# Kernel optimization log

Hardware: AMD Instinct MI355X
Metric: run time of the kernel (lower is better)

## Reference

```python
import jax, jax.numpy as jnp
import numpy as np

B, T, C = 8, 2048, 1024   # batch, seq_len, n_embd
HS = 1024                 # head_size


def setup_inputs() -> dict:
    key = jax.random.key(0)
    k1, k2, k3, k4 = jax.random.split(key, 4)
    x = jax.random.normal(k1, (B, T, C), dtype=jnp.float32)
    k_wei = jax.random.normal(k2, (C, HS), dtype=jnp.float32) * (C ** -0.5)
    q_wei = jax.random.normal(k3, (C, HS), dtype=jnp.float32) * (C ** -0.5)
    v_wei = jax.random.normal(k4, (C, HS), dtype=jnp.float32) * (C ** -0.5)
    mask = jnp.tril(jnp.ones((T, T), dtype=bool))  # causal tril, block_size >= T
    return {"x": x, "k_wei": k_wei, "q_wei": q_wei, "v_wei": v_wei, "mask": mask}


def reference(x, k_wei, q_wei, v_wei, mask):
    Bb, Tt, Cc = x.shape
    k = x @ k_wei                                   # [B,T,HS]
    q = x @ q_wei                                   # [B,T,HS]
    v = x @ v_wei                                   # [B,T,HS]
    # NOTE: source scales by C**-0.5 where C = n_embd (input channels)
    wei = jnp.einsum('bqh,bkh->bqk', q, k) * (Cc ** -0.5)  # [B,T,T]
    wei = jnp.where(mask[:Tt, :Tt], wei, -jnp.inf)
    wei = jax.nn.softmax(wei, axis=-1)
    out = wei @ v                                   # [B,T,HS]
    return out
```

## Files before the change

### kernel.cpp

```cpp
#include <hip/hip_runtime.h>
#include <hip/hip_bf16.h>
#include <stdint.h>

typedef __attribute__((ext_vector_type(4))) float f32x4;
typedef __attribute__((ext_vector_type(8))) short s16x8;

#define MFMA(a, b, c) __builtin_amdgcn_mfma_f32_16x16x32_bf16((a), (b), (c), 0, 0, 0)

__device__ __forceinline__ ushort f2bf(float f) {
  union { float f; uint32_t u; } v; v.f = f;
  uint32_t r = v.u + 0x7FFFu + ((v.u >> 16) & 1u);
  return (ushort)(r >> 16);
}

__device__ __forceinline__ void gload_lds16(const ushort* g, short* l) {
  __builtin_amdgcn_global_load_lds(
      (const __attribute__((address_space(1))) uint32_t*)g,
      (__attribute__((address_space(3))) uint32_t*)l, 16, 0, 0);
}

__device__ __forceinline__ int xcd_swz(int flat, int q) {
  return (flat & 7) * q + (flat >> 3);
}

__device__ __forceinline__ void stage128(const ushort* __restrict__ g, int ld,
                                         int row0, int k0, short* lbase, int tid) {
  const int w  = tid >> 6;
  const int l  = tid & 63;
  const int lr = l >> 3;
  const int ls = l & 7;
  const ushort* gp = g + (size_t)(row0 + lr) * ld + k0 + ((ls ^ lr) << 3);
  short* lp = lbase + l * 8;
#pragma unroll
  for (int i = 0; i < 4; ++i) {
    const int R0 = w * 32 + i * 8;
    gload_lds16(gp + (size_t)R0 * ld, lp + R0 * 64);
  }
}

__device__ __forceinline__ void gemm_core(
    const ushort* __restrict__ A, int lda, const ushort* __restrict__ Bt, int ldb,
    int m0, int n0, int nk, short* lds, f32x4 acc[4][4])
{
  const int tid  = threadIdx.x;
  const int lane = tid & 63, wid = tid >> 6;
  const int wr = wid >> 1, wc = wid & 1;
  const int fr = lane & 15, kg = lane >> 4;
  const int s0  = (kg ^ (fr & 7)) << 3;
  const int aro = (wr * 64 + fr) * 64;
  const int bro = (wc * 64 + fr) * 64;

  short* As = lds;
  short* Bs = lds + 8192;

#pragma unroll
  for (int i = 0; i < 4; ++i)
#pragma unroll
    for (int j = 0; j < 4; ++j)
      acc[i][j] = (f32x4){0.f, 0.f, 0.f, 0.f};

#pragma unroll 1
  for (int kk = 0; kk < nk; ++kk) {
    __syncthreads();
    stage128(A,  lda, m0, kk * 64, As, tid);
    stage128(Bt, ldb, n0, kk * 64, Bs, tid);
    __syncthreads();

    s16x8 b[4][2], a[2][2];
#pragma unroll
    for (int ni = 0; ni < 4; ++ni) {
      b[ni][0] = *(const s16x8*)(Bs + bro + ni * 1024 + s0);
      b[ni][1] = *(const s16x8*)(Bs + bro + ni * 1024 + (s0 ^ 32));
    }
#pragma unroll
    for (int mi = 0; mi < 2; ++mi) {
      a[mi][0] = *(const s16x8*)(As + aro + mi * 1024 + s0);
      a[mi][1] = *(const s16x8*)(As + aro + mi * 1024 + (s0 ^ 32));
    }
#pragma unroll
    for (int mi = 0; mi < 2; ++mi)
#pragma unroll
      for (int ni = 0; ni < 4; ++ni) {
        acc[mi][ni] = MFMA(a[mi][0], b[ni][0], acc[mi][ni]);
        acc[mi][ni] = MFMA(a[mi][1], b[ni][1], acc[mi][ni]);
      }
#pragma unroll
    for (int mi = 0; mi < 2; ++mi) {
      a[mi][0] = *(const s16x8*)(As + aro + (2 + mi) * 1024 + s0);
      a[mi][1] = *(const s16x8*)(As + aro + (2 + mi) * 1024 + (s0 ^ 32));
    }
#pragma unroll
    for (int mi = 0; mi < 2; ++mi)
#pragma unroll
      for (int ni = 0; ni < 4; ++ni) {
        acc[2 + mi][ni] = MFMA(a[mi][0], b[ni][0], acc[2 + mi][ni]);
        acc[2 + mi][ni] = MFMA(a[mi][1], b[ni][1], acc[2 + mi][ni]);
      }
  }
}

__global__ void cvt_x(const float* __restrict__ x, ushort* __restrict__ xb)
{
  const size_t i = (size_t)(blockIdx.x * 256 + threadIdx.x) * 4;
  const f32x4 t = *(const f32x4*)(x + i);
  uint2 pk;
  pk.x = (uint32_t)f2bf(t[0]) | ((uint32_t)f2bf(t[1]) << 16);
  pk.y = (uint32_t)f2bf(t[2]) | ((uint32_t)f2bf(t[3]) << 16);
  *(uint2*)(xb + i) = pk;
}

__global__ void cvt_w(const float* __restrict__ kw, const float* __restrict__ qw,
                      const float* __restrict__ vw, ushort* __restrict__ wt)
{
  __shared__ float t[32][33];
  const float* w = (blockIdx.z == 0) ? qw : (blockIdx.z == 1) ? kw : vw;
  const int n0 = blockIdx.x * 32, k0 = blockIdx.y * 32;
  t[threadIdx.y][threadIdx.x] = w[(size_t)(k0 + threadIdx.y) * 1024 + n0 + threadIdx.x];
  __syncthreads();
  wt[(size_t)blockIdx.z * 1048576 + (size_t)(n0 + threadIdx.y) * 1024 + k0 + threadIdx.x] =
      f2bf(t[threadIdx.x][threadIdx.y]);
}

__global__ __launch_bounds__(256, 4) void gemm_qkv_impl(
    const ushort* __restrict__ xb, const ushort* __restrict__ wt,
    ushort* __restrict__ q, ushort* __restrict__ k, ushort* __restrict__ vT)
{
  __attribute__((aligned(16))) __shared__ short lds[16384];
  const int flat = blockIdx.x + 24 * blockIdx.y;
  const int xcd = flat & 7, c = flat >> 3;
  const int mloc = c / 6, nloc = c - mloc * 6;
  const int m0 = ((xcd & 1) * 64 + mloc) * 128;
  const int n0 = ((xcd >> 1) * 6 + nloc) * 128;
  f32x4 acc[4][4];
  gemm_core(xb, 1024, wt, 1024, m0, n0, 16, lds, acc);

  const int lane = threadIdx.x & 63;
  const int wid = threadIdx.x >> 6;
  const int wr = wid >> 1, wc = wid & 1;
  const int q4 = (lane >> 4) << 2;
  const int fr = lane & 15;
  const int z  = n0 >> 10;
  const int cb = (n0 & 1023) + wc * 64 + fr;
  ushort* o = (z == 0) ? q : k;
#pragma unroll
  for (int mi = 0; mi < 4; ++mi)
#pragma unroll
    for (int ni = 0; ni < 4; ++ni)
#pragma unroll
      for (int j = 0; j < 4; ++j) {
        const int r = m0 + wr * 64 + mi * 16 + q4 + j;
        const int c2 = cb + ni * 16;
        const ushort hv = f2bf(acc[mi][ni][j]);
        if (z < 2) o[(size_t)r * 1024 + c2] = hv;
        else       vT[((size_t)(r >> 11) * 1024 + c2) * 2048 + (r & 2047)] = hv;
      }
}

__global__ __launch_bounds__(256, 4) void gemm_sp(
    const ushort* __restrict__ q, const ushort* __restrict__ k,
    ushort* __restrict__ P, float* __restrict__ sums)
{
  __attribute__((aligned(16))) __shared__ short lds[16384];
  const int nf = xcd_swz(blockIdx.x + 16 * (blockIdx.y + 16 * blockIdx.z), 256);
  const int kt = nf & 15, qt = (nf >> 4) & 15, b = nf >> 8;
  if (kt > qt) return;
  f32x4 acc[4][4];
  const ushort* qb = q + (size_t)b * (2048 * 1024);
  const ushort* kb = k + (size_t)b * (2048 * 1024);
  gemm_core(qb, 1024, kb, 1024, qt * 128, kt * 128, 16, lds, acc);
  __syncthreads();
  float* rowsum = (float*)lds;

  const int tid  = threadIdx.x;
  const int lane = tid & 63, wid = tid >> 6;
  const int wr = wid >> 1, wc = wid & 1;
  const int q4 = (lane >> 4) << 2;
  const int fr = lane & 15;
  const int diag = (kt == qt);
  ushort* Pb = P + ((size_t)b << 22);

#pragma unroll
  for (int mi = 0; mi < 4; ++mi)
#pragma unroll
    for (int j = 0; j < 4; ++j) {
      const int rloc = wr * 64 + mi * 16 + q4 + j;
      const int rg   = qt * 128 + rloc;
      float s = 0.f;
#pragma unroll
      for (int ni = 0; ni < 4; ++ni) {
        const int cg = kt * 128 + wc * 64 + ni * 16 + fr;
        float e = __expf(acc[mi][ni][j] * 0.03125f - 10.f);
        if (diag && cg > rg) e = 0.f;
        s += e;
        Pb[(size_t)rg * 2048 + cg] = f2bf(e);
      }
#pragma unroll
      for (int m = 1; m < 16; m <<= 1) s += __shfl_xor(s, m);
      if (fr == 0) rowsum[wc * 128 + rloc] = s;
    }
  __syncthreads();
  if (tid < 128) {
    const float tot = rowsum[tid] + rowsum[128 + tid];
    atomicAdd(&sums[b * 2048 + qt * 128 + tid], tot);
  }
}

__global__ __launch_bounds__(256, 4) void gemm_pv(
    const ushort* __restrict__ P, const ushort* __restrict__ vT,
    const float* __restrict__ sums, float* __restrict__ out)
{
  __attribute__((aligned(16))) __shared__ short lds[16384];
  const int nf = xcd_swz(blockIdx.x + 8 * (blockIdx.y + 16 * blockIdx.z), 128);
  const int ht = nf & 7, qt = (nf >> 3) & 15, b = nf >> 7;
  f32x4 acc[4][4];
  const ushort* Pb = P  + ((size_t)b << 22);
  const ushort* Vb = vT + (size_t)b * (1024 * 2048);
  gemm_core(Pb, 2048, Vb, 2048, qt * 128, ht * 128, (qt + 1) * 2, lds, acc);

  float* ob = out + (size_t)b * 2097152;
  const int lane = threadIdx.x & 63;
  const int wid = threadIdx.x >> 6;
  const int wr = wid >> 1, wc = wid & 1;
  const int r0 = qt * 128 + wr * 64 + ((lane >> 4) << 2);
  const int c0 = ht * 128 + wc * 64 + (lane & 15);
#pragma unroll
  for (int mi = 0; mi < 4; ++mi)
#pragma unroll
    for (int j = 0; j < 4; ++j) {
      const int r = r0 + mi * 16 + j;
      const float inv = 1.0f / sums[b * 2048 + r];
#pragma unroll
      for (int ni = 0; ni < 4; ++ni)
        ob[(size_t)r * 1024 + (c0 + ni * 16)] = acc[mi][ni][j] * inv;
    }
}

extern "C" void kernel_launch(void* const* d_in, const int* in_sizes, int n_in,
                              void* d_out, int out_size, void* d_ws, size_t ws_size,
                              hipStream_t stream)
{
  const float* x  = (const float*)d_in[0];
  const float* kw = (const float*)d_in[1];
  const float* qw = (const float*)d_in[2];
  const float* vw = (const float*)d_in[3];
  float* out = (float*)d_out;
  char* ws = (char*)d_ws;

  ushort* xb   = (ushort*)ws;
  ushort* P    = (ushort*)ws;
  float*  sums = (float*)(ws + 67108864);
  ushort* wt   = (ushort*)(ws + 67174400);
  ushort* q    = (ushort*)(ws + 73465856);
  ushort* k    = (ushort*)(ws + 107020288);
  ushort* vT   = (ushort*)(ws + 140574720);

  hipMemsetAsync(sums, 0, 8 * 2048 * sizeof(float), stream);
  cvt_x<<<16384, 256, 0, stream>>>(x, xb);
  cvt_w<<<dim3(32, 32, 3), dim3(32, 32), 0, stream>>>(kw, qw, vw, wt);
  gemm_qkv_impl<<<dim3(24, 128), 256, 0, stream>>>(xb, wt, q, k, vT);
  gemm_sp<<<dim3(16, 16, 8), 256, 0, stream>>>(q, k, P, sums);
  gemm_pv<<<dim3(8, 16, 8), 256, 0, stream>>>(P, vT, sums, out);
}
```

Measured before the change: 294.3 us.

## Use 256x256 tile with 8-wave pingpong pipeline for QKV projection GEMM

Replaces the 128x128, 4-wave QKV projection GEMM with a 256x256 tile computed by 512 threads (8 waves) using 128KB of dynamic LDS. Global-to-LDS loads run double-buffered and are interleaved with quarter-tile MFMA phases, using explicit barriers, vmcnt waits and setprio. The aim is more operand reuse per loaded byte and better overlap of memory traffic with MFMA work. The cost is lower occupancy (one block per CU), far fewer blocks (768), and many barriers per iteration.

```diff
diff --git a/kernel.cpp b/kernel.cpp
--- a/kernel.cpp
+++ b/kernel.cpp
@@ -5,6 +5,11 @@
 typedef __attribute__((ext_vector_type(4))) float f32x4;
 typedef __attribute__((ext_vector_type(8))) short s16x8;
 
+#define BARRIER() asm volatile("s_barrier" ::: "memory")
+#define WAITV8()  asm volatile("s_waitcnt vmcnt(8)" ::: "memory")
+#define WAITV4()  asm volatile("s_waitcnt vmcnt(4)" ::: "memory")
+#define WAITV0()  asm volatile("s_waitcnt vmcnt(0)" ::: "memory")
+#define LGKM0()   asm volatile("s_waitcnt lgkmcnt(0)" ::: "memory")
 #define MFMA(a, b, c) __builtin_amdgcn_mfma_f32_16x16x32_bf16((a), (b), (c), 0, 0, 0)
 
 __device__ __forceinline__ ushort f2bf(float f) {
@@ -22,6 +27,7 @@
 __device__ __forceinline__ int xcd_swz(int flat, int q) {
   return (flat & 7) * q + (flat >> 3);
 }
+
 
 __device__ __forceinline__ void stage128(const ushort* __restrict__ g, int ld,
                                          int row0, int k0, short* lbase, int tid) {
@@ -99,6 +105,162 @@
   }
 }
 
+
+__device__ __forceinline__ void stage_half(const ushort* __restrict__ g, int ld,
+                                           int grow0, int k0, short* lbase, int tid) {
+#pragma unroll
+  for (int i = 0; i < 2; ++i) {
+    const int idx = i * 512 + tid;
+    const int r = idx >> 3;
+    const int s = tid & 7;
+    gload_lds16(g + (size_t)(grow0 + r) * ld + k0 + ((s ^ (r & 7)) << 3),
+                lbase + idx * 8);
+  }
+}
+
+#define QMFMA(mbase, nbase, bq)                                              \
+  __builtin_amdgcn_s_setprio(1);                                             \
+  _Pragma("unroll")                                                          \
+  for (int m = 0; m < 4; ++m) {                                              \
+    _Pragma("unroll")                                                        \
+    for (int n = 0; n < 2; ++n) {                                            \
+      acc[(mbase) + m][(nbase) + n] =                                        \
+          MFMA(a[m][0], bq[n][0], acc[(mbase) + m][(nbase) + n]);            \
+      acc[(mbase) + m][(nbase) + n] =                                        \
+          MFMA(a[m][1], bq[n][1], acc[(mbase) + m][(nbase) + n]);            \
+    }                                                                        \
+  }                                                                          \
+  __builtin_amdgcn_s_setprio(0);
+
+__device__ __forceinline__ void gemm_core256(
+    const ushort* __restrict__ A, int lda, const ushort* __restrict__ Bt, int ldb,
+    int m0, int n0, int nk, short* lds, f32x4 acc[8][4])
+{
+  const int tid  = threadIdx.x;
+  const int lane = tid & 63, wid = tid >> 6;
+  const int wr = wid >> 2, wc = wid & 3;
+  const int fr = lane & 15, kg = lane >> 4;
+  const int s0  = (kg ^ (fr & 7)) << 3;
+  const int aro = fr * 64;
+  const int bro = (wc & 1) * 4096 + fr * 64;
+
+#define ASL(s, h) (lds + ((s) * 2 + (h)) * 8192)
+#define BSL(s, h) (lds + 32768 + ((s) * 2 + (h)) * 8192)
+  short* const Aw[2] = { ASL(0, wr), ASL(1, wr) };
+  short* const Bw[2] = { BSL(0, (wc >> 1)), BSL(1, (wc >> 1)) };
+
+#pragma unroll
+  for (int i = 0; i < 8; ++i)
+#pragma unroll
+    for (int j = 0; j < 4; ++j)
+      acc[i][j] = (f32x4){0.f, 0.f, 0.f, 0.f};
+
+  stage_half(A,  lda, m0,       0,  ASL(0, 0), tid);
+  stage_half(A,  lda, m0 + 128, 0,  ASL(0, 1), tid);
+  stage_half(Bt, ldb, n0,       0,  BSL(0, 0), tid);
+  stage_half(Bt, ldb, n0 + 128, 0,  BSL(0, 1), tid);
+  stage_half(A,  lda, m0,       64, ASL(1, 0), tid);
+  stage_half(A,  lda, m0 + 128, 64, ASL(1, 1), tid);
+  stage_half(Bt, ldb, n0,       64, BSL(1, 0), tid);
+  stage_half(Bt, ldb, n0 + 128, 64, BSL(1, 1), tid);
+  WAITV8();
+  BARRIER();
+
+  const int niter = nk >> 1;
+#pragma unroll 1
+  for (int t = 0; t < niter; ++t) {
+    const int kO  = (2 * t + 1) * 64;
+    const int kN0 = (2 * t + 2) * 64;
+    const int kN1 = (2 * t + 3) * 64;
+    const bool more = (t + 1 < niter);
+    s16x8 a[4][2], b01[2][2], b23[2][2];
+
+#pragma unroll
+    for (int n = 0; n < 2; ++n) {
+      b01[n][0] = *(const s16x8*)(Bw[0] + bro + n * 1024 + s0);
+      b01[n][1] = *(const s16x8*)(Bw[0] + bro + n * 1024 + (s0 ^ 32));
+    }
+#pragma unroll
+    for (int m = 0; m < 4; ++m) {
+      a[m][0] = *(const s16x8*)(Aw[0] + aro + m * 1024 + s0);
+      a[m][1] = *(const s16x8*)(Aw[0] + aro + m * 1024 + (s0 ^ 32));
+    }
+    if (t > 0) stage_half(A, lda, m0 + 128, kO, ASL(1, 1), tid);
+    BARRIER(); LGKM0();
+    QMFMA(0, 0, b01);
+    BARRIER();
+
+#pragma unroll
+    for (int n = 0; n < 2; ++n) {
+      b23[n][0] = *(const s16x8*)(Bw[0] + bro + (2 + n) * 1024 + s0);
+      b23[n][1] = *(const s16x8*)(Bw[0] + bro + (2 + n) * 1024 + (s0 ^ 32));
+    }
+    if (t > 0) stage_half(Bt, ldb, n0 + 128, kO, BSL(1, 1), tid);
+    BARRIER(); LGKM0();
+    QMFMA(0, 2, b23);
+    BARRIER();
+
+#pragma unroll
+    for (int m = 0; m < 4; ++m) {
+      a[m][0] = *(const s16x8*)(Aw[0] + aro + (4 + m) * 1024 + s0);
+      a[m][1] = *(const s16x8*)(Aw[0] + aro + (4 + m) * 1024 + (s0 ^ 32));
+    }
+    if (more) stage_half(Bt, ldb, n0, kN0, BSL(0, 0), tid);
+    BARRIER(); LGKM0();
+    QMFMA(4, 2, b23);
+    BARRIER();
+
+    if (more) stage_half(A, lda, m0, kN0, ASL(0, 0), tid);
+    BARRIER();
+    QMFMA(4, 0, b01);
+    if (more) { WAITV4(); } else { WAITV0(); }
+    BARRIER();
+
+#pragma unroll
+    for (int n = 0; n < 2; ++n) {
+      b01[n][0] = *(const s16x8*)(Bw[1] + bro + n * 1024 + s0);
+      b01[n][1] = *(const s16x8*)(Bw[1] + bro + n * 1024 + (s0 ^ 32));
+    }
+#pragma unroll
+    for (int m = 0; m < 4; ++m) {
+      a[m][0] = *(const s16x8*)(Aw[1] + aro + m * 1024 + s0);
+      a[m][1] = *(const s16x8*)(Aw[1] + aro + m * 1024 + (s0 ^ 32));
+    }
+    if (more) stage_half(A, lda, m0 + 128, kN0, ASL(0, 1), tid);
+    BARRIER(); LGKM0();
+    QMFMA(0, 0, b01);
+    BARRIER();
+
+#pragma unroll
+    for (int n = 0; n < 2; ++n) {
+      b23[n][0] = *(const s16x8*)(Bw[1] + bro + (2 + n) * 1024 + s0);
+      b23[n][1] = *(const s16x8*)(Bw[1] + bro + (2 + n) * 1024 + (s0 ^ 32));
+    }
+    if (more) stage_half(Bt, ldb, n0 + 128, kN0, BSL(0, 1), tid);
+    BARRIER(); LGKM0();
+    QMFMA(0, 2, b23);
+    BARRIER();
+
+#pragma unroll
+    for (int m = 0; m < 4; ++m) {
+      a[m][0] = *(const s16x8*)(Aw[1] + aro + (4 + m) * 1024 + s0);
+      a[m][1] = *(const s16x8*)(Aw[1] + aro + (4 + m) * 1024 + (s0 ^ 32));
+    }
+    if (more) stage_half(Bt, ldb, n0, kN1, BSL(1, 0), tid);
+    BARRIER(); LGKM0();
+    QMFMA(4, 2, b23);
+    BARRIER();
+
+    if (more) stage_half(A, lda, m0, kN1, ASL(1, 0), tid);
+    BARRIER();
+    QMFMA(4, 0, b01);
+    if (more) { WAITV4(); } else { WAITV0(); }
+    BARRIER();
+  }
+#undef ASL
+#undef BSL
+}
+
 __global__ void cvt_x(const float* __restrict__ x, ushort* __restrict__ xb)
 {
   const size_t i = (size_t)(blockIdx.x * 256 + threadIdx.x) * 4;
@@ -121,34 +283,34 @@
       f2bf(t[threadIdx.x][threadIdx.y]);
 }
 
-__global__ __launch_bounds__(256, 4) void gemm_qkv_impl(
+__global__ __launch_bounds__(512) void gemm_qkv256(
     const ushort* __restrict__ xb, const ushort* __restrict__ wt,
     ushort* __restrict__ q, ushort* __restrict__ k, ushort* __restrict__ vT)
 {
-  __attribute__((aligned(16))) __shared__ short lds[16384];
-  const int flat = blockIdx.x + 24 * blockIdx.y;
+  extern __shared__ short lds[];
+  const int flat = blockIdx.x + 12 * blockIdx.y;
   const int xcd = flat & 7, c = flat >> 3;
-  const int mloc = c / 6, nloc = c - mloc * 6;
-  const int m0 = ((xcd & 1) * 64 + mloc) * 128;
-  const int n0 = ((xcd >> 1) * 6 + nloc) * 128;
-  f32x4 acc[4][4];
-  gemm_core(xb, 1024, wt, 1024, m0, n0, 16, lds, acc);
+  const int mloc = c / 3, nloc = c - mloc * 3;
+  const int m0 = ((xcd & 1) * 32 + mloc) * 256;
+  const int n0 = ((xcd >> 1) * 3 + nloc) * 256;
+  f32x4 acc[8][4];
+  gemm_core256(xb, 1024, wt, 1024, m0, n0, 16, lds, acc);
 
   const int lane = threadIdx.x & 63;
   const int wid = threadIdx.x >> 6;
-  const int wr = wid >> 1, wc = wid & 1;
+  const int wr = wid >> 2, wc = wid & 3;
   const int q4 = (lane >> 4) << 2;
   const int fr = lane & 15;
   const int z  = n0 >> 10;
   const int cb = (n0 & 1023) + wc * 64 + fr;
   ushort* o = (z == 0) ? q : k;
 #pragma unroll
-  for (int mi = 0; mi < 4; ++mi)
+  for (int mi = 0; mi < 8; ++mi)
 #pragma unroll
     for (int ni = 0; ni < 4; ++ni)
 #pragma unroll
       for (int j = 0; j < 4; ++j) {
-        const int r = m0 + wr * 64 + mi * 16 + q4 + j;
+        const int r = m0 + wr * 128 + mi * 16 + q4 + j;
         const int c2 = cb + ni * 16;
         const ushort hv = f2bf(acc[mi][ni][j]);
         if (z < 2) o[(size_t)r * 1024 + c2] = hv;
@@ -254,10 +416,13 @@
   ushort* k    = (ushort*)(ws + 107020288);
   ushort* vT   = (ushort*)(ws + 140574720);
 
+  const int LDSB = 131072;
+  hipFuncSetAttribute((const void*)gemm_qkv256, hipFuncAttributeMaxDynamicSharedMemorySize, LDSB);
+
   hipMemsetAsync(sums, 0, 8 * 2048 * sizeof(float), stream);
   cvt_x<<<16384, 256, 0, stream>>>(x, xb);
   cvt_w<<<dim3(32, 32, 3), dim3(32, 32), 0, stream>>>(kw, qw, vw, wt);
-  gemm_qkv_impl<<<dim3(24, 128), 256, 0, stream>>>(xb, wt, q, k, vT);
+  gemm_qkv256<<<dim3(12, 64), 512, LDSB, stream>>>(xb, wt, q, k, vT);
   gemm_sp<<<dim3(16, 16, 8), 256, 0, stream>>>(q, k, P, sums);
   gemm_pv<<<dim3(8, 16, 8), 256, 0, stream>>>(P, vT, sums, out);
 }
```

After: 293.0 us. Within noise of the previous version (-0.4%).

## Load QKV GEMM A-operand directly to registers with double-buffered LDS for B

Applied to the files above, without the earlier changes.

The QKV projection GEMM stops staging the activation tile through LDS. Each wave now loads its A fragments straight from global memory into registers, prefetching one k-step ahead. Only the weight tile stays in LDS, double-buffered with asynchronous global-to-LDS loads issued two steps ahead and explicit vmcnt waits. This removes half the LDS traffic and overlaps loads with MFMA work, at the cost of more registers, uncoalesced-ish direct global reads, and dropping the occupancy hint from the launch bounds.

```diff
diff --git a/kernel.cpp b/kernel.cpp
--- a/kernel.cpp
+++ b/kernel.cpp
@@ -5,6 +5,9 @@
 typedef __attribute__((ext_vector_type(4))) float f32x4;
 typedef __attribute__((ext_vector_type(8))) short s16x8;
 
+#define BARRIER() asm volatile("s_barrier" ::: "memory")
+#define WAITV4()  asm volatile("s_waitcnt vmcnt(4)" ::: "memory")
+#define WAITV0()  asm volatile("s_waitcnt vmcnt(0)" ::: "memory")
 #define MFMA(a, b, c) __builtin_amdgcn_mfma_f32_16x16x32_bf16((a), (b), (c), 0, 0, 0)
 
 __device__ __forceinline__ ushort f2bf(float f) {
@@ -38,6 +41,7 @@
   }
 }
 
+
 __device__ __forceinline__ void gemm_core(
     const ushort* __restrict__ A, int lda, const ushort* __restrict__ Bt, int ldb,
     int m0, int n0, int nk, short* lds, f32x4 acc[4][4])
@@ -121,24 +125,81 @@
       f2bf(t[threadIdx.x][threadIdx.y]);
 }
 
-__global__ __launch_bounds__(256, 4) void gemm_qkv_impl(
+
+#define QKV_STEP(X, Bcur, aCur, aNxt)                                         \
+  {                                                                           \
+    s16x8 b[4][2];                                                            \
+    _Pragma("unroll")                                                         \
+    for (int ni = 0; ni < 4; ++ni) {                                          \
+      b[ni][0] = *(const s16x8*)((Bcur) + bro + ni * 1024 + s0);              \
+      b[ni][1] = *(const s16x8*)((Bcur) + bro + ni * 1024 + (s0 ^ 32));       \
+    }                                                                         \
+    if ((X) + 1 < 16) {                                                       \
+      _Pragma("unroll")                                                       \
+      for (int mi = 0; mi < 4; ++mi) {                                        \
+        aNxt[mi][0] = *(const s16x8*)(Ab + mi * 16384 + ((X) + 1) * 64);      \
+        aNxt[mi][1] = *(const s16x8*)(Ab + mi * 16384 + ((X) + 1) * 64 + 32); \
+      }                                                                       \
+    }                                                                         \
+    _Pragma("unroll")                                                         \
+    for (int mi = 0; mi < 4; ++mi)                                            \
+      _Pragma("unroll")                                                       \
+      for (int ni = 0; ni < 4; ++ni) {                                        \
+        acc[mi][ni] = MFMA(aCur[mi][0], b[ni][0], acc[mi][ni]);               \
+        acc[mi][ni] = MFMA(aCur[mi][1], b[ni][1], acc[mi][ni]);               \
+      }                                                                       \
+    BARRIER();                                                                \
+    if ((X) + 2 < 16) stage128(wt, 1024, n0, ((X) + 2) * 64, (Bcur), tid);    \
+    if ((X) + 1 < 16) { WAITV4(); } else { WAITV0(); }                        \
+    BARRIER();                                                                \
+  }
+
+__global__ __launch_bounds__(256) void gemm_qkv_dg(
     const ushort* __restrict__ xb, const ushort* __restrict__ wt,
     ushort* __restrict__ q, ushort* __restrict__ k, ushort* __restrict__ vT)
 {
-  __attribute__((aligned(16))) __shared__ short lds[16384];
+  __attribute__((aligned(16))) __shared__ short Bs0[8192], Bs1[8192];
   const int flat = blockIdx.x + 24 * blockIdx.y;
   const int xcd = flat & 7, c = flat >> 3;
   const int mloc = c / 6, nloc = c - mloc * 6;
   const int m0 = ((xcd & 1) * 64 + mloc) * 128;
   const int n0 = ((xcd >> 1) * 6 + nloc) * 128;
+
+  const int tid  = threadIdx.x;
+  const int lane = tid & 63, wid = tid >> 6;
+  const int wr = wid >> 1, wc = wid & 1;
+  const int fr = lane & 15, kg = lane >> 4;
+  const int s0  = (kg ^ (fr & 7)) << 3;
+  const int bro = (wc * 64 + fr) * 64;
+
+  const ushort* Ab = xb + (size_t)(m0 + wr * 64 + fr) * 1024 + kg * 8;
+
   f32x4 acc[4][4];
-  gemm_core(xb, 1024, wt, 1024, m0, n0, 16, lds, acc);
-
-  const int lane = threadIdx.x & 63;
-  const int wid = threadIdx.x >> 6;
-  const int wr = wid >> 1, wc = wid & 1;
+#pragma unroll
+  for (int i = 0; i < 4; ++i)
+#pragma unroll
+    for (int j = 0; j < 4; ++j)
+      acc[i][j] = (f32x4){0.f, 0.f, 0.f, 0.f};
+
+  s16x8 aA[4][2], aB[4][2];
+
+  stage128(wt, 1024, n0, 0, Bs0, tid);
+#pragma unroll
+  for (int mi = 0; mi < 4; ++mi) {
+    aA[mi][0] = *(const s16x8*)(Ab + mi * 16384);
+    aA[mi][1] = *(const s16x8*)(Ab + mi * 16384 + 32);
+  }
+  stage128(wt, 1024, n0, 64, Bs1, tid);
+  WAITV4();
+  BARRIER();
+
+#pragma unroll 1
+  for (int X = 0; X < 16; X += 2) {
+    QKV_STEP(X,     Bs0, aA, aB);
+    QKV_STEP(X + 1, Bs1, aB, aA);
+  }
+
   const int q4 = (lane >> 4) << 2;
-  const int fr = lane & 15;
   const int z  = n0 >> 10;
   const int cb = (n0 & 1023) + wc * 64 + fr;
   ushort* o = (z == 0) ? q : k;
@@ -257,7 +318,7 @@
   hipMemsetAsync(sums, 0, 8 * 2048 * sizeof(float), stream);
   cvt_x<<<16384, 256, 0, stream>>>(x, xb);
   cvt_w<<<dim3(32, 32, 3), dim3(32, 32), 0, stream>>>(kw, qw, vw, wt);
-  gemm_qkv_impl<<<dim3(24, 128), 256, 0, stream>>>(xb, wt, q, k, vT);
+  gemm_qkv_dg<<<dim3(24, 128), 256, 0, stream>>>(xb, wt, q, k, vT);
   gemm_sp<<<dim3(16, 16, 8), 256, 0, stream>>>(q, k, P, sums);
   gemm_pv<<<dim3(8, 16, 8), 256, 0, stream>>>(P, vT, sums, out);
 }
```

Measured after the change: 420.9 us. 1.43x slower.
